# Kernel tuning notes

Hardware: AMD Instinct MI355X
Metric: run time of the kernel (lower is better)

## Reference

```python
import jax, jax.numpy as jnp
import numpy as np

N = 100000
E = 1600000
IN_DIM = 256
HID = 256
OUT = 64
K = 10
ALPHA = 0.1


def setup_inputs() -> dict:
    key = jax.random.key(0)
    ks = jax.random.split(key, 8)
    x = jax.random.normal(ks[0], (N, IN_DIM), dtype=jnp.float32)
    edge_index = jax.random.randint(ks[1], (2, E), 0, N, dtype=jnp.int64)
    # Linear params (torch default-ish scale)
    W1 = jax.random.normal(ks[2], (IN_DIM, HID), dtype=jnp.float32) / np.sqrt(IN_DIM)
    b1 = jnp.zeros((HID,), dtype=jnp.float32)
    W2 = jax.random.normal(ks[3], (HID, OUT), dtype=jnp.float32) / np.sqrt(HID)
    b2 = jnp.zeros((OUT,), dtype=jnp.float32)
    alpha = jnp.asarray([ALPHA * (1.0 - ALPHA) ** k for k in range(K + 1)], dtype=jnp.float32)
    return {"x": x, "edge_index": edge_index, "W1": W1, "b1": b1, "W2": W2, "b2": b2, "alpha": alpha}


def reference(x, edge_index, W1, b1, W2, b2, alpha):
    # MLP head (dropout = identity in eval)
    h = jax.nn.relu(x @ W1 + b1) @ W2 + b2  # [N, OUT]

    row, col = edge_index[0], edge_index[1]
    num_nodes = h.shape[0]
    # degree over row (matches torch_geometric degree(row, ...))
    deg = jax.ops.segment_sum(jnp.ones_like(row, dtype=h.dtype), row, num_segments=num_nodes)
    deg_inv_sqrt = jnp.where(deg > 0, jax.lax.rsqrt(jnp.maximum(deg, 1.0)), 0.0)
    norm = deg_inv_sqrt[row] * deg_inv_sqrt[col]  # [E]

    gamma = jax.nn.softmax(alpha)

    def step(carry, g):
        h_cur, acc = carry
        msg = h_cur[col] * norm[:, None]  # gather + scale  [E, OUT]
        h_new = jax.ops.segment_sum(msg, row, num_segments=num_nodes)  # scatter_add
        return (h_new, acc + g * h_new), None

    acc0 = gamma[0] * h
    (_, out), _ = jax.lax.scan(step, (h, acc0), gamma[1:])
    return out
```

## Files before the change

kernel.cpp:

```cpp
#include <hip/hip_runtime.h>
#include <hip/hip_bf16.h>

#define N_NODES 100000
#define N_EDGES 1600000
#define IN_DIM_ 256
#define HID_ 256
#define OUT_ 64
#define KSTEPS 10

typedef __attribute__((ext_vector_type(4))) float f32x4;
typedef __attribute__((ext_vector_type(8))) __bf16 bf16x8;
typedef __attribute__((ext_vector_type(8))) unsigned short u16x8;

static __device__ __forceinline__ unsigned short f2bf(float f) {
    union { float f; unsigned int u; } v; v.f = f;
    unsigned int u = v.u;
    unsigned int r = u + 0x7FFFu + ((u >> 16) & 1u);
    return (unsigned short)(r >> 16);
}
static __device__ __forceinline__ float bflo(unsigned int v) {
    return __uint_as_float(v << 16);
}
static __device__ __forceinline__ float bfhi(unsigned int v) {
    return __uint_as_float(v & 0xFFFF0000u);
}


__global__ void gamma_kernel(const float* __restrict__ alpha, float* __restrict__ gamma) {
    if (threadIdx.x == 0) {
        float m = alpha[0];
        for (int i = 1; i <= KSTEPS; ++i) m = fmaxf(m, alpha[i]);
        float e[KSTEPS + 1];
        float s = 0.f;
        for (int i = 0; i <= KSTEPS; ++i) { e[i] = expf(alpha[i] - m); s += e[i]; }
        float inv = 1.f / s;
        for (int i = 0; i <= KSTEPS; ++i) gamma[i] = e[i] * inv;
    }
}

__global__ void deg_kernel(const int* __restrict__ row, int* __restrict__ deg, int E) {
    int e = blockIdx.x * 256 + threadIdx.x;
    if (e < E) atomicAdd(&deg[row[e]], 1);
}

__global__ void dis_kernel(const int* __restrict__ deg, float* __restrict__ dis, int n) {
    int i = blockIdx.x * 256 + threadIdx.x;
    if (i < n) {
        int d = deg[i];
        dis[i] = d > 0 ? rsqrtf((float)d) : 0.f;
    }
}

__global__ void wcast_kernel(const float* __restrict__ W, unsigned short* __restrict__ wT,
                             int K, int N) {
    int k = blockIdx.x * 256 + threadIdx.x;
    int n = blockIdx.y;
    if (k < K) wT[(size_t)n * K + k] = f2bf(W[(size_t)k * N + n]);
}

__global__ __launch_bounds__(256) void xcast_kernel(const float* __restrict__ x,
                                                    unsigned short* __restrict__ xb, int n8) {
    int i = blockIdx.x * 256 + threadIdx.x;
    if (i < n8) {
        const float* p = x + (size_t)i * 8;
        u16x8 v;
        #pragma unroll
        for (int j = 0; j < 8; ++j) v[j] = f2bf(p[j]);
        *(u16x8*)&xb[(size_t)i * 8] = v;
    }
}


__global__ __launch_bounds__(256) void scan_sum_kernel(const int* __restrict__ deg,
                                                       int* __restrict__ bsum, int n) {
    __shared__ int s[256];
    int t = threadIdx.x;
    int i = blockIdx.x * 256 + t;
    s[t] = (i < n) ? deg[i] : 0;
    __syncthreads();
    for (int st = 128; st > 0; st >>= 1) {
        if (t < st) s[t] += s[t + st];
        __syncthreads();
    }
    if (t == 0) bsum[blockIdx.x] = s[0];
}

__global__ __launch_bounds__(512) void scan_block_kernel(int* __restrict__ bsum,
                                                         int* __restrict__ off,
                                                         int nblk, int n) {
    __shared__ int s[512];
    int t = threadIdx.x;
    int v = (t < nblk) ? bsum[t] : 0;
    s[t] = v;
    __syncthreads();
    for (int st = 1; st < 512; st <<= 1) {
        int a = (t >= st) ? s[t - st] : 0;
        __syncthreads();
        s[t] += a;
        __syncthreads();
    }
    if (t < nblk) bsum[t] = s[t] - v;
    if (t == 511) off[n] = s[511];
}

__global__ __launch_bounds__(256) void scan_final_kernel(const int* __restrict__ deg,
                                                         const int* __restrict__ bsum,
                                                         int* __restrict__ off, int n) {
    __shared__ int s[256];
    int t = threadIdx.x;
    int i = blockIdx.x * 256 + t;
    int v = (i < n) ? deg[i] : 0;
    s[t] = v;
    __syncthreads();
    for (int st = 1; st < 256; st <<= 1) {
        int a = (t >= st) ? s[t - st] : 0;
        __syncthreads();
        s[t] += a;
        __syncthreads();
    }
    if (i < n) off[i] = bsum[blockIdx.x] + s[t] - v;
}

__global__ void csr_scatter_kernel(const int* __restrict__ row, const int* __restrict__ col,
                                   const float* __restrict__ dis, const int* __restrict__ off,
                                   int* __restrict__ cursor, int2* __restrict__ ecsr, int E) {
    int e = blockIdx.x * 256 + threadIdx.x;
    if (e < E) {
        int r = row[e], c = col[e];
        float w = dis[r] * dis[c];
        int pos = atomicAdd(&cursor[r], 1);
        int2 p;
        p.x = c;
        p.y = __float_as_int(w);
        ecsr[(size_t)off[r] + pos] = p;
    }
}

__global__ __launch_bounds__(512) void gemm1_kernel(const unsigned short* __restrict__ xb,
                                                    const unsigned short* __restrict__ w1T,
                                                    const float* __restrict__ b1,
                                                    unsigned short* __restrict__ h1, int M) {
    __shared__ unsigned short As[128][40];
    __shared__ unsigned short Bs[256][40];

    const int tid = threadIdx.x;
    const int lane = tid & 63;
    const int w = tid >> 6;
    const int wr = w >> 1, wc = w & 1;
    const int row0 = blockIdx.x * 128;

    const int am = tid >> 2;
    const int ak = (tid & 3) * 8;
    const int bn = tid >> 1;
    const int bh = (tid & 1) * 16;
    const int fr = lane & 15;
    const int ko = (lane >> 4) * 8;

    f32x4 acc[2][8] = {};

    for (int kk = 0; kk < 256; kk += 32) {
        {
            int gr = row0 + am;
            if (gr < M) {
                *(u16x8*)&As[am][ak] = *(const u16x8*)&xb[(size_t)gr * IN_DIM_ + kk + ak];
            } else {
                u16x8 z = {};
                *(u16x8*)&As[am][ak] = z;
            }
        }
        {
            const unsigned short* p = &w1T[(size_t)bn * 256 + kk + bh];
            *(u16x8*)&Bs[bn][bh]     = *(const u16x8*)&p[0];
            *(u16x8*)&Bs[bn][bh + 8] = *(const u16x8*)&p[8];
        }
        __syncthreads();

        bf16x8 a[2];
        #pragma unroll
        for (int mi = 0; mi < 2; ++mi) a[mi] = *(const bf16x8*)&As[wr * 32 + mi * 16 + fr][ko];
        #pragma unroll
        for (int ni = 0; ni < 8; ++ni) {
            bf16x8 b = *(const bf16x8*)&Bs[wc * 128 + ni * 16 + fr][ko];
            #pragma unroll
            for (int mi = 0; mi < 2; ++mi)
                acc[mi][ni] = __builtin_amdgcn_mfma_f32_16x16x32_bf16(a[mi], b, acc[mi][ni], 0, 0, 0);
        }
        __syncthreads();
    }

    const int rg = (lane >> 4) * 4;
    #pragma unroll
    for (int mi = 0; mi < 2; ++mi) {
        #pragma unroll
        for (int r = 0; r < 4; ++r) {
            int gm = row0 + wr * 32 + mi * 16 + rg + r;
            if (gm < M) {
                #pragma unroll
                for (int ni = 0; ni < 8; ++ni) {
                    int gn = wc * 128 + ni * 16 + fr;
                    float v = acc[mi][ni][r] + b1[gn];
                    v = fmaxf(v, 0.f);
                    h1[(size_t)gm * HID_ + gn] = f2bf(v);
                }
            }
        }
    }
}

__global__ __launch_bounds__(256) void gemm2_kernel(const unsigned short* __restrict__ h1,
                                                    const unsigned short* __restrict__ w2T,
                                                    const float* __restrict__ b2,
                                                    const float* __restrict__ gamma,
                                                    unsigned short* __restrict__ h,
                                                    float* __restrict__ out, int M) {
    __shared__ unsigned short As[64][40];
    __shared__ unsigned short Bs[64][40];

    const int tid = threadIdx.x;
    const int lane = tid & 63;
    const int w = tid >> 6;
    const int wr = w >> 1, wc = w & 1;
    const int row0 = blockIdx.x * 64;

    const int am = tid >> 2;
    const int ak = (tid & 3) * 8;
    const int fr = lane & 15;
    const int ko = (lane >> 4) * 8;

    f32x4 acc[2][2] = {};

    for (int kk = 0; kk < 256; kk += 32) {
        {
            int gr = row0 + am;
            if (gr < M) {
                *(u16x8*)&As[am][ak] = *(const u16x8*)&h1[(size_t)gr * HID_ + kk + ak];
            } else {
                u16x8 z = {};
                *(u16x8*)&As[am][ak] = z;
            }
        }
        if (tid < 128) {
            int n = tid >> 1, hf = (tid & 1) * 16;
            const unsigned short* p = &w2T[(size_t)n * 256 + kk + hf];
            *(u16x8*)&Bs[n][hf]     = *(const u16x8*)&p[0];
            *(u16x8*)&Bs[n][hf + 8] = *(const u16x8*)&p[8];
        }
        __syncthreads();

        bf16x8 a[2], b[2];
        #pragma unroll
        for (int mi = 0; mi < 2; ++mi) a[mi] = *(const bf16x8*)&As[wr * 32 + mi * 16 + fr][ko];
        #pragma unroll
        for (int ni = 0; ni < 2; ++ni) b[ni] = *(const bf16x8*)&Bs[wc * 32 + ni * 16 + fr][ko];
        #pragma unroll
        for (int mi = 0; mi < 2; ++mi)
            #pragma unroll
            for (int ni = 0; ni < 2; ++ni)
                acc[mi][ni] = __builtin_amdgcn_mfma_f32_16x16x32_bf16(a[mi], b[ni], acc[mi][ni], 0, 0, 0);
        __syncthreads();
    }

    const float g0 = gamma[0];
    const int rg = (lane >> 4) * 4;
    #pragma unroll
    for (int mi = 0; mi < 2; ++mi) {
        #pragma unroll
        for (int r = 0; r < 4; ++r) {
            int gm = row0 + wr * 32 + mi * 16 + rg + r;
            if (gm < M) {
                #pragma unroll
                for (int ni = 0; ni < 2; ++ni) {
                    int gn = wc * 32 + ni * 16 + fr;
                    float v = acc[mi][ni][r] + b2[gn];
                    h[(size_t)gm * OUT_ + gn] = f2bf(v);
                    out[(size_t)gm * OUT_ + gn] = g0 * v;
                }
            }
        }
    }
}

__global__ __launch_bounds__(256) void pull_kernel(const int* __restrict__ off,
                                                   const int2* __restrict__ ecsr,
                                                   const unsigned short* __restrict__ hc,
                                                   unsigned short* __restrict__ hn,
                                                   float* __restrict__ out,
                                                   const float* __restrict__ gamma,
                                                   int k, int fuse, int n) {
    int node = blockIdx.x * 4 + (threadIdx.x >> 6);
    if (node >= n) return;
    int lane = threadIdx.x & 63;
    int half = lane >> 5;
    int fl = (lane & 31) * 2;
    int s = off[node], e = off[node + 1];
    float acc0 = 0.f, acc1 = 0.f;

    int j = s + half;
    for (; j + 14 < e; j += 16) {
        int2 p0 = ecsr[j],      p1 = ecsr[j + 2],  p2 = ecsr[j + 4],  p3 = ecsr[j + 6];
        int2 p4 = ecsr[j + 8],  p5 = ecsr[j + 10], p6 = ecsr[j + 12], p7 = ecsr[j + 14];
        unsigned int v0 = *(const unsigned int*)&hc[(size_t)p0.x * OUT_ + fl];
        unsigned int v1 = *(const unsigned int*)&hc[(size_t)p1.x * OUT_ + fl];
        unsigned int v2 = *(const unsigned int*)&hc[(size_t)p2.x * OUT_ + fl];
        unsigned int v3 = *(const unsigned int*)&hc[(size_t)p3.x * OUT_ + fl];
        unsigned int v4 = *(const unsigned int*)&hc[(size_t)p4.x * OUT_ + fl];
        unsigned int v5 = *(const unsigned int*)&hc[(size_t)p5.x * OUT_ + fl];
        unsigned int v6 = *(const unsigned int*)&hc[(size_t)p6.x * OUT_ + fl];
        unsigned int v7 = *(const unsigned int*)&hc[(size_t)p7.x * OUT_ + fl];
        float w0 = __int_as_float(p0.y), w1 = __int_as_float(p1.y);
        float w2 = __int_as_float(p2.y), w3 = __int_as_float(p3.y);
        float w4 = __int_as_float(p4.y), w5 = __int_as_float(p5.y);
        float w6 = __int_as_float(p6.y), w7 = __int_as_float(p7.y);
        acc0 += w0 * bflo(v0); acc1 += w0 * bfhi(v0);
        acc0 += w1 * bflo(v1); acc1 += w1 * bfhi(v1);
        acc0 += w2 * bflo(v2); acc1 += w2 * bfhi(v2);
        acc0 += w3 * bflo(v3); acc1 += w3 * bfhi(v3);
        acc0 += w4 * bflo(v4); acc1 += w4 * bfhi(v4);
        acc0 += w5 * bflo(v5); acc1 += w5 * bfhi(v5);
        acc0 += w6 * bflo(v6); acc1 += w6 * bfhi(v6);
        acc0 += w7 * bflo(v7); acc1 += w7 * bfhi(v7);
    }
    for (; j + 2 < e; j += 4) {
        int2 pa = ecsr[j], pb = ecsr[j + 2];
        unsigned int va = *(const unsigned int*)&hc[(size_t)pa.x * OUT_ + fl];
        unsigned int vb = *(const unsigned int*)&hc[(size_t)pb.x * OUT_ + fl];
        float wa = __int_as_float(pa.y), wb = __int_as_float(pb.y);
        acc0 += wa * bflo(va); acc1 += wa * bfhi(va);
        acc0 += wb * bflo(vb); acc1 += wb * bfhi(vb);
    }
    if (j < e) {
        int2 p = ecsr[j];
        unsigned int v = *(const unsigned int*)&hc[(size_t)p.x * OUT_ + fl];
        float w = __int_as_float(p.y);
        acc0 += w * bflo(v);
        acc1 += w * bfhi(v);
    }

    acc0 += __shfl_xor(acc0, 32);
    acc1 += __shfl_xor(acc1, 32);

    if (lane < 32) {
        size_t o = (size_t)node * OUT_ + fl;
        if (k < KSTEPS) {
            unsigned int packed = (unsigned int)f2bf(acc0) | ((unsigned int)f2bf(acc1) << 16);
            *(unsigned int*)&hn[o] = packed;
        }
        if (fuse) {
            float gp = gamma[k - 1], gc = gamma[k];
            unsigned int hown = *(const unsigned int*)&hc[o];
            float2* op = (float2*)&out[o];
            float2 ov = *op;
            ov.x += gp * bflo(hown) + gc * acc0;
            ov.y += gp * bfhi(hown) + gc * acc1;
            *op = ov;
        }
    }
}

extern "C" void kernel_launch(void* const* d_in, const int* in_sizes, int n_in,
                              void* d_out, int out_size, void* d_ws, size_t ws_size,
                              hipStream_t stream) {
    const float* x = (const float*)d_in[0];
    const int* ei = (const int*)d_in[1];
    const float* W1 = (const float*)d_in[2];
    const float* b1 = (const float*)d_in[3];
    const float* W2 = (const float*)d_in[4];
    const float* b2 = (const float*)d_in[5];
    const float* alpha = (const float*)d_in[6];
    const int* row = ei;
    const int* col = ei + N_EDGES;
    float* out = (float*)d_out;

    const int NBLK = (N_NODES + 255) / 256;

    char* wsb = (char*)d_ws;
    size_t p = 0;
    auto alloc = [&](size_t bytes) { size_t r = p; p += (bytes + 255) & ~255ull; return r; };
    float* gamma = (float*)(wsb + alloc(16 * 4));
    int* off     = (int*)(wsb + alloc((N_NODES + 1) * 4));
    int* cursor  = (int*)(wsb + alloc(N_NODES * 4));
    int* deg     = (int*)(wsb + alloc(N_NODES * 4));
    float* dis   = (float*)(wsb + alloc(N_NODES * 4));
    int* bsum    = (int*)(wsb + alloc(512 * 4));
    unsigned short* w1T = (unsigned short*)(wsb + alloc((size_t)IN_DIM_ * HID_ * 2));
    unsigned short* w2T = (unsigned short*)(wsb + alloc((size_t)HID_ * OUT_ * 2));
    int2* ecsr   = (int2*)(wsb + alloc((size_t)N_EDGES * 8));
    unsigned short* xb  = (unsigned short*)(wsb + alloc((size_t)N_NODES * IN_DIM_ * 2));
    unsigned short* h1  = (unsigned short*)(wsb + alloc((size_t)N_NODES * HID_ * 2));
    unsigned short* h_a = (unsigned short*)(wsb + alloc((size_t)N_NODES * OUT_ * 2));
    unsigned short* h_b = h1;

    hipMemsetAsync(cursor, 0, N_NODES * sizeof(int), stream);
    hipMemsetAsync(deg, 0, N_NODES * sizeof(int), stream);
    gamma_kernel<<<1, 64, 0, stream>>>(alpha, gamma);
    deg_kernel<<<(N_EDGES + 255) / 256, 256, 0, stream>>>(row, deg, N_EDGES);
    dis_kernel<<<NBLK, 256, 0, stream>>>(deg, dis, N_NODES);
    scan_sum_kernel<<<NBLK, 256, 0, stream>>>(deg, bsum, N_NODES);
    scan_block_kernel<<<1, 512, 0, stream>>>(bsum, off, NBLK, N_NODES);
    scan_final_kernel<<<NBLK, 256, 0, stream>>>(deg, bsum, off, N_NODES);
    csr_scatter_kernel<<<(N_EDGES + 255) / 256, 256, 0, stream>>>(row, col, dis, off, cursor,
                                                                  ecsr, N_EDGES);
    wcast_kernel<<<dim3(1, HID_), 256, 0, stream>>>(W1, w1T, IN_DIM_, HID_);
    wcast_kernel<<<dim3(1, OUT_), 256, 0, stream>>>(W2, w2T, HID_, OUT_);
    xcast_kernel<<<(N_NODES * IN_DIM_ / 8 + 255) / 256, 256, 0, stream>>>(
        x, xb, N_NODES * IN_DIM_ / 8);

    gemm1_kernel<<<(N_NODES + 127) / 128, 512, 0, stream>>>(xb, w1T, b1, h1, N_NODES);
    gemm2_kernel<<<(N_NODES + 63) / 64, 256, 0, stream>>>(h1, w2T, b2, gamma, h_a, out, N_NODES);

    unsigned short* hc = h_a;
    unsigned short* hn = h_b;
    for (int k = 1; k <= KSTEPS; ++k) {
        int fuse = (k % 2 == 0);
        pull_kernel<<<(N_NODES + 3) / 4, 256, 0, stream>>>(off, ecsr, hc, hn, out, gamma, k,
                                                           fuse, N_NODES);
        unsigned short* t = hc; hc = hn; hn = t;
    }
}
```

Baseline: 788.7 us.

## Factor symmetric edge norm into per-node scaling to halve CSR edge storage

The symmetric normalization dis[r]*dis[c] is split so that features are pre-scaled by dis at the source and post-scaled by dis at the destination. The CSR edge array then stores only column indices (4 bytes instead of 8), which cuts edge-stream traffic in each propagation step and removes per-edge multiplies. The output accumulation is now done every step rather than fused every other step, which adds an out read-modify-write in the odd steps. Storing dis-scaled values in bf16 slightly changes rounding behaviour.

```diff
diff --git a/kernel.cpp b/kernel.cpp
--- a/kernel.cpp
+++ b/kernel.cpp
@@ -122,17 +122,13 @@
 }
 
 __global__ void csr_scatter_kernel(const int* __restrict__ row, const int* __restrict__ col,
-                                   const float* __restrict__ dis, const int* __restrict__ off,
-                                   int* __restrict__ cursor, int2* __restrict__ ecsr, int E) {
+                                   const int* __restrict__ off,
+                                   int* __restrict__ cursor, int* __restrict__ ecsr, int E) {
     int e = blockIdx.x * 256 + threadIdx.x;
     if (e < E) {
-        int r = row[e], c = col[e];
-        float w = dis[r] * dis[c];
+        int r = row[e];
         int pos = atomicAdd(&cursor[r], 1);
-        int2 p;
-        p.x = c;
-        p.y = __float_as_int(w);
-        ecsr[(size_t)off[r] + pos] = p;
+        ecsr[(size_t)off[r] + pos] = col[e];
     }
 }
 
@@ -211,7 +207,8 @@
                                                     const unsigned short* __restrict__ w2T,
                                                     const float* __restrict__ b2,
                                                     const float* __restrict__ gamma,
-                                                    unsigned short* __restrict__ h,
+                                                    const float* __restrict__ dis,
+                                                    unsigned short* __restrict__ g,
                                                     float* __restrict__ out, int M) {
     __shared__ unsigned short As[64][40];
     __shared__ unsigned short Bs[64][40];
@@ -268,11 +265,12 @@
         for (int r = 0; r < 4; ++r) {
             int gm = row0 + wr * 32 + mi * 16 + rg + r;
             if (gm < M) {
+                float dr = dis[gm];
                 #pragma unroll
                 for (int ni = 0; ni < 2; ++ni) {
                     int gn = wc * 32 + ni * 16 + fr;
                     float v = acc[mi][ni][r] + b2[gn];
-                    h[(size_t)gm * OUT_ + gn] = f2bf(v);
+                    g[(size_t)gm * OUT_ + gn] = f2bf(dr * v);
                     out[(size_t)gm * OUT_ + gn] = g0 * v;
                 }
             }
@@ -281,12 +279,13 @@
 }
 
 __global__ __launch_bounds__(256) void pull_kernel(const int* __restrict__ off,
-                                                   const int2* __restrict__ ecsr,
-                                                   const unsigned short* __restrict__ hc,
-                                                   unsigned short* __restrict__ hn,
+                                                   const int* __restrict__ ecsr,
+                                                   const float* __restrict__ dis,
+                                                   const unsigned short* __restrict__ gc,
+                                                   unsigned short* __restrict__ gn,
                                                    float* __restrict__ out,
                                                    const float* __restrict__ gamma,
-                                                   int k, int fuse, int n) {
+                                                   int k, int n) {
     int node = blockIdx.x * 4 + (threadIdx.x >> 6);
     if (node >= n) return;
     int lane = threadIdx.x & 63;
@@ -297,63 +296,57 @@
 
     int j = s + half;
     for (; j + 14 < e; j += 16) {
-        int2 p0 = ecsr[j],      p1 = ecsr[j + 2],  p2 = ecsr[j + 4],  p3 = ecsr[j + 6];
-        int2 p4 = ecsr[j + 8],  p5 = ecsr[j + 10], p6 = ecsr[j + 12], p7 = ecsr[j + 14];
-        unsigned int v0 = *(const unsigned int*)&hc[(size_t)p0.x * OUT_ + fl];
-        unsigned int v1 = *(const unsigned int*)&hc[(size_t)p1.x * OUT_ + fl];
-        unsigned int v2 = *(const unsigned int*)&hc[(size_t)p2.x * OUT_ + fl];
-        unsigned int v3 = *(const unsigned int*)&hc[(size_t)p3.x * OUT_ + fl];
-        unsigned int v4 = *(const unsigned int*)&hc[(size_t)p4.x * OUT_ + fl];
-        unsigned int v5 = *(const unsigned int*)&hc[(size_t)p5.x * OUT_ + fl];
-        unsigned int v6 = *(const unsigned int*)&hc[(size_t)p6.x * OUT_ + fl];
-        unsigned int v7 = *(const unsigned int*)&hc[(size_t)p7.x * OUT_ + fl];
-        float w0 = __int_as_float(p0.y), w1 = __int_as_float(p1.y);
-        float w2 = __int_as_float(p2.y), w3 = __int_as_float(p3.y);
-        float w4 = __int_as_float(p4.y), w5 = __int_as_float(p5.y);
-        float w6 = __int_as_float(p6.y), w7 = __int_as_float(p7.y);
-        acc0 += w0 * bflo(v0); acc1 += w0 * bfhi(v0);
-        acc0 += w1 * bflo(v1); acc1 += w1 * bfhi(v1);
-        acc0 += w2 * bflo(v2); acc1 += w2 * bfhi(v2);
-        acc0 += w3 * bflo(v3); acc1 += w3 * bfhi(v3);
-        acc0 += w4 * bflo(v4); acc1 += w4 * bfhi(v4);
-        acc0 += w5 * bflo(v5); acc1 += w5 * bfhi(v5);
-        acc0 += w6 * bflo(v6); acc1 += w6 * bfhi(v6);
-        acc0 += w7 * bflo(v7); acc1 += w7 * bfhi(v7);
+        int c0 = ecsr[j],      c1 = ecsr[j + 2],  c2 = ecsr[j + 4],  c3 = ecsr[j + 6];
+        int c4 = ecsr[j + 8],  c5 = ecsr[j + 10], c6 = ecsr[j + 12], c7 = ecsr[j + 14];
+        unsigned int v0 = *(const unsigned int*)&gc[(size_t)c0 * OUT_ + fl];
+        unsigned int v1 = *(const unsigned int*)&gc[(size_t)c1 * OUT_ + fl];
+        unsigned int v2 = *(const unsigned int*)&gc[(size_t)c2 * OUT_ + fl];
+        unsigned int v3 = *(const unsigned int*)&gc[(size_t)c3 * OUT_ + fl];
+        unsigned int v4 = *(const unsigned int*)&gc[(size_t)c4 * OUT_ + fl];
+        unsigned int v5 = *(const unsigned int*)&gc[(size_t)c5 * OUT_ + fl];
+        unsigned int v6 = *(const unsigned int*)&gc[(size_t)c6 * OUT_ + fl];
+        unsigned int v7 = *(const unsigned int*)&gc[(size_t)c7 * OUT_ + fl];
+        acc0 += bflo(v0); acc1 += bfhi(v0);
+        acc0 += bflo(v1); acc1 += bfhi(v1);
+        acc0 += bflo(v2); acc1 += bfhi(v2);
+        acc0 += bflo(v3); acc1 += bfhi(v3);
+        acc0 += bflo(v4); acc1 += bfhi(v4);
+        acc0 += bflo(v5); acc1 += bfhi(v5);
+        acc0 += bflo(v6); acc1 += bfhi(v6);
+        acc0 += bflo(v7); acc1 += bfhi(v7);
     }
     for (; j + 2 < e; j += 4) {
-        int2 pa = ecsr[j], pb = ecsr[j + 2];
-        unsigned int va = *(const unsigned int*)&hc[(size_t)pa.x * OUT_ + fl];
-        unsigned int vb = *(const unsigned int*)&hc[(size_t)pb.x * OUT_ + fl];
-        float wa = __int_as_float(pa.y), wb = __int_as_float(pb.y);
-        acc0 += wa * bflo(va); acc1 += wa * bfhi(va);
-        acc0 += wb * bflo(vb); acc1 += wb * bfhi(vb);
+        int ca = ecsr[j], cb = ecsr[j + 2];
+        unsigned int va = *(const unsigned int*)&gc[(size_t)ca * OUT_ + fl];
+        unsigned int vb = *(const unsigned int*)&gc[(size_t)cb * OUT_ + fl];
+        acc0 += bflo(va); acc1 += bfhi(va);
+        acc0 += bflo(vb); acc1 += bfhi(vb);
     }
     if (j < e) {
-        int2 p = ecsr[j];
-        unsigned int v = *(const unsigned int*)&hc[(size_t)p.x * OUT_ + fl];
-        float w = __int_as_float(p.y);
-        acc0 += w * bflo(v);
-        acc1 += w * bfhi(v);
+        int c = ecsr[j];
+        unsigned int v = *(const unsigned int*)&gc[(size_t)c * OUT_ + fl];
+        acc0 += bflo(v);
+        acc1 += bfhi(v);
     }
 
     acc0 += __shfl_xor(acc0, 32);
     acc1 += __shfl_xor(acc1, 32);
 
     if (lane < 32) {
+        float dr = dis[node];
+        float h0 = dr * acc0, h1v = dr * acc1;
         size_t o = (size_t)node * OUT_ + fl;
         if (k < KSTEPS) {
-            unsigned int packed = (unsigned int)f2bf(acc0) | ((unsigned int)f2bf(acc1) << 16);
-            *(unsigned int*)&hn[o] = packed;
-        }
-        if (fuse) {
-            float gp = gamma[k - 1], gc = gamma[k];
-            unsigned int hown = *(const unsigned int*)&hc[o];
-            float2* op = (float2*)&out[o];
-            float2 ov = *op;
-            ov.x += gp * bflo(hown) + gc * acc0;
-            ov.y += gp * bfhi(hown) + gc * acc1;
-            *op = ov;
-        }
+            unsigned int packed = (unsigned int)f2bf(dr * h0) |
+                                  ((unsigned int)f2bf(dr * h1v) << 16);
+            *(unsigned int*)&gn[o] = packed;
+        }
+        float gk = gamma[k];
+        float2* op = (float2*)&out[o];
+        float2 ov = *op;
+        ov.x += gk * h0;
+        ov.y += gk * h1v;
+        *op = ov;
     }
 }
 
@@ -384,11 +377,11 @@
     int* bsum    = (int*)(wsb + alloc(512 * 4));
     unsigned short* w1T = (unsigned short*)(wsb + alloc((size_t)IN_DIM_ * HID_ * 2));
     unsigned short* w2T = (unsigned short*)(wsb + alloc((size_t)HID_ * OUT_ * 2));
-    int2* ecsr   = (int2*)(wsb + alloc((size_t)N_EDGES * 8));
+    int* ecsr    = (int*)(wsb + alloc((size_t)N_EDGES * 4));
     unsigned short* xb  = (unsigned short*)(wsb + alloc((size_t)N_NODES * IN_DIM_ * 2));
     unsigned short* h1  = (unsigned short*)(wsb + alloc((size_t)N_NODES * HID_ * 2));
-    unsigned short* h_a = (unsigned short*)(wsb + alloc((size_t)N_NODES * OUT_ * 2));
-    unsigned short* h_b = h1;
+    unsigned short* g_a = (unsigned short*)(wsb + alloc((size_t)N_NODES * OUT_ * 2));
+    unsigned short* g_b = h1;
 
     hipMemsetAsync(cursor, 0, N_NODES * sizeof(int), stream);
     hipMemsetAsync(deg, 0, N_NODES * sizeof(int), stream);
@@ -398,7 +391,7 @@
     scan_sum_kernel<<<NBLK, 256, 0, stream>>>(deg, bsum, N_NODES);
     scan_block_kernel<<<1, 512, 0, stream>>>(bsum, off, NBLK, N_NODES);
     scan_final_kernel<<<NBLK, 256, 0, stream>>>(deg, bsum, off, N_NODES);
-    csr_scatter_kernel<<<(N_EDGES + 255) / 256, 256, 0, stream>>>(row, col, dis, off, cursor,
+    csr_scatter_kernel<<<(N_EDGES + 255) / 256, 256, 0, stream>>>(row, col, off, cursor,
                                                                   ecsr, N_EDGES);
     wcast_kernel<<<dim3(1, HID_), 256, 0, stream>>>(W1, w1T, IN_DIM_, HID_);
     wcast_kernel<<<dim3(1, OUT_), 256, 0, stream>>>(W2, w2T, HID_, OUT_);
@@ -406,14 +399,14 @@
         x, xb, N_NODES * IN_DIM_ / 8);
 
     gemm1_kernel<<<(N_NODES + 127) / 128, 512, 0, stream>>>(xb, w1T, b1, h1, N_NODES);
-    gemm2_kernel<<<(N_NODES + 63) / 64, 256, 0, stream>>>(h1, w2T, b2, gamma, h_a, out, N_NODES);
-
-    unsigned short* hc = h_a;
-    unsigned short* hn = h_b;
+    gemm2_kernel<<<(N_NODES + 63) / 64, 256, 0, stream>>>(h1, w2T, b2, gamma, dis, g_a, out,
+                                                          N_NODES);
+
+    unsigned short* gc = g_a;
+    unsigned short* gn = g_b;
     for (int k = 1; k <= KSTEPS; ++k) {
-        int fuse = (k % 2 == 0);
-        pull_kernel<<<(N_NODES + 3) / 4, 256, 0, stream>>>(off, ecsr, hc, hn, out, gamma, k,
-                                                           fuse, N_NODES);
-        unsigned short* t = hc; hc = hn; hn = t;
-    }
-}
+        pull_kernel<<<(N_NODES + 3) / 4, 256, 0, stream>>>(off, ecsr, dis, gc, gn, out, gamma,
+                                                           k, N_NODES);
+        unsigned short* t = gc; gc = gn; gn = t;
+    }
+}
```

After: 787.4 us. About the same (-0.2%).
